# Kernel tuning notes

Measured on AMD Instinct MI355X. Metric: run time of the kernel, lower is better.

## Reference

```python
import math
import jax, jax.numpy as jnp
import numpy as np

IN_SIZE = 16
OUT_SIZE = 16
MIN_SCALE = 1e-3
CONST = 1000.0
DEFAULT_U_A = math.log(math.e - 1.0 - MIN_SCALE)
BATCH = 32768
N_PARAMS = OUT_SIZE ** 2 + 2 * OUT_SIZE + OUT_SIZE * IN_SIZE  # 544


def setup_inputs() -> dict:
    key = jax.random.key(0)
    kx, kh = jax.random.split(key)
    x = jax.random.normal(kx, (BATCH, IN_SIZE), dtype=jnp.float32)
    h = jax.random.normal(kh, (BATCH, N_PARAMS), dtype=jnp.float32)
    return {"x": x, "h": h}


def reference(x, h):
    B = h.shape[0]
    O, I = OUT_SIZE, IN_SIZE
    # extract_parameters
    da = h[:, :O]                                   # (B,O)
    db = h[:, O:2 * O]                              # (B,O)
    dw = h[:, 2 * O:2 * O + O * O].reshape(B, O, O)  # (B,O,O)
    du = h[:, 2 * O + O * O:].reshape(B, O, I)       # (B,O,I)

    u_pre = du / CONST
    u = jax.nn.softmax(u_pre, axis=-1)
    log_u = jax.nn.log_softmax(u_pre, axis=-1)
    a = jax.nn.softplus(DEFAULT_U_A + da / CONST) + MIN_SCALE
    b = db / CONST
    w_pre = dw / CONST
    w = jax.nn.softmax(w_pre, axis=-1)
    log_w = jax.nn.log_softmax(w_pre, axis=-1)

    # forward transform
    ux = jnp.einsum('boi,bi->bo', u, x)             # (B,O)
    c = jax.nn.sigmoid(a * ux + b)                  # (B,O)
    d = jnp.einsum('bij,bj->bi', w, c)              # (B,O)
    z = jnp.log(d / (1.0 - d))                      # inverse_sigmoid

    # log-space Jacobian: J = diag(1/(d(1-d))) @ W @ diag(sigma'(c)*a) @ U
    log_t1 = (jnp.log(d) - jnp.log(1.0 - d))[:, :, None]                  # (B,O,1)
    log_t3 = (jax.nn.log_sigmoid(c) + jax.nn.log_sigmoid(-c))[:, None, :]  # (B,1,O)
    log_t4 = jnp.log(a)[:, None, :]                                        # (B,1,O)
    m1 = (log_t1 + log_w + log_t3 + log_t4)[:, :, :, None]                 # (B,O,O,1)
    m2 = log_u[:, None, :, :]                                              # (B,1,O,I)
    # log_dot: logsumexp over the contraction dim (-2), keepdim
    log_jac = jax.scipy.special.logsumexp(m1 + m2, axis=-2, keepdims=True)  # (B,O,1,I)
    log_det = jnp.sum(log_jac, axis=(1, 2, 3))                              # (B,)
    return z, log_det


if __name__ == "__main__":
    out = reference(**setup_inputs())
    print(out[0].shape, out[1].shape)
```

## Files before the change

### kernel.cpp

```cpp
#include <hip/hip_runtime.h>

#define BATCH   32768
#define OSZ     16
#define ISZ     16
#define NP      544
#define EPB     16
#define HS      552
#define NF4     (EPB*NP/4)
#define ROWF4   (NP/4)

__global__ __launch_bounds__(256, 4)
void dsit_kernel(const float* __restrict__ x, const float* __restrict__ h,
                 float* __restrict__ out_z, float* __restrict__ out_ld) {
    __shared__ float h_s[EPB * HS];
    __shared__ float x_s[EPB * ISZ];
    __shared__ float c_s[EPB * OSZ];
    __shared__ float s_s[EPB * OSZ];

    const int tid = threadIdx.x;
    const int blk = blockIdx.x;

    {
        const float4* hg = (const float4*)(h + (size_t)blk * (EPB * NP));
        #pragma unroll
        for (int k = 0; k < 9; ++k) {
            int f4 = tid + (k << 8);
            if (f4 < NF4) {
                int e  = f4 / ROWF4;
                int c4 = f4 - e * ROWF4;
                ((float4*)h_s)[e * (HS / 4) + c4] = hg[f4];
            }
        }
        if (tid < (EPB * ISZ / 4)) {
            ((float4*)x_s)[tid] = ((const float4*)(x + (size_t)blk * (EPB * ISZ)))[tid];
        }
    }
    __syncthreads();

    const int e = tid >> 4;
    const int r = tid & 15;
    float* he = &h_s[e * HS];
    const float* xe = &x_s[e * ISZ];

    const float K = 1.0e-3f;
    const float u_a = logf(expf(1.0f) - 1.001f);

    float a  = log1pf(expf(u_a + he[r] * K)) + 1.0e-3f;
    float bb = he[OSZ + r] * K;

    float wrow[16];
    float wsum = 0.0f;
    #pragma unroll
    for (int j = 0; j < 16; ++j) {
        float v = __expf(he[32 + 16 * r + j] * K);
        wrow[j] = v; wsum += v;
    }
    float winv = 1.0f / wsum;
    #pragma unroll
    for (int j = 0; j < 16; ++j) wrow[j] *= winv;

    float urow[16];
    float usum = 0.0f;
    #pragma unroll
    for (int i = 0; i < 16; ++i) {
        float v = __expf(he[288 + 16 * r + i] * K);
        urow[i] = v; usum += v;
    }
    float uinv = 1.0f / usum;
    float ux = 0.0f;
    #pragma unroll
    for (int i = 0; i < 16; ++i) {
        urow[i] *= uinv;
        ux += urow[i] * xe[i];
    }
    #pragma unroll
    for (int i = 0; i < 16; ++i) he[288 + 16 * r + i] = urow[i];

    float cpre = a * ux + bb;
    float c  = 1.0f / (1.0f + __expf(-cpre));
    float sc = 1.0f / (1.0f + __expf(-c));
    float s  = sc * (1.0f - sc) * a;
    c_s[e * OSZ + r] = c;
    s_s[e * OSZ + r] = s;
    __syncthreads();

    float d = 0.0f;
    #pragma unroll
    for (int j = 0; j < 16; ++j) d += wrow[j] * c_s[e * OSZ + j];
    float z = logf(d) - logf(1.0f - d);
    out_z[(size_t)blk * 256 + tid] = z;

    #pragma unroll
    for (int j = 0; j < 16; ++j) wrow[j] *= s_s[e * OSZ + j];

    float acc[16];
    #pragma unroll
    for (int i = 0; i < 16; ++i) acc[i] = 0.0f;
    #pragma unroll
    for (int j = 0; j < 16; ++j) {
        float wj = wrow[j];
        const float* uj = &he[288 + 16 * j];
        #pragma unroll
        for (int i = 0; i < 16; ++i) acc[i] += wj * uj[i];
    }

    float partial = 16.0f * z;
    #pragma unroll
    for (int i = 0; i < 16; ++i) partial += logf(acc[i]);

    #pragma unroll
    for (int m = 1; m < 16; m <<= 1) partial += __shfl_xor(partial, m, 16);
    if (r == 0) out_ld[blk * EPB + e] = partial;
}

extern "C" void kernel_launch(void* const* d_in, const int* in_sizes, int n_in,
                              void* d_out, int out_size, void* d_ws, size_t ws_size,
                              hipStream_t stream) {
    const float* x = (const float*)d_in[0];
    const float* h = (const float*)d_in[1];
    float* out_z  = (float*)d_out;
    float* out_ld = out_z + (size_t)BATCH * OSZ;

    dim3 grid(BATCH / EPB);
    dim3 block(256);
    dsit_kernel<<<grid, block, 0, stream>>>(x, h, out_z, out_ld);
}
```

Measured before the change: 108.8 us.

## Load h rows straight from global into registers and shrink shared memory

Each thread now reads its own U and W rows from global memory as float4 loads into registers, where the old kernel first staged the whole 544-float parameter block in shared memory. Only the normalized U rows go to a smaller padded shared buffer, and c and s are packed into one float2 array. The Jacobian contraction reads U as float4 from shared memory, and the exact logf/log1pf calls are replaced with __logf. The aim is less shared-memory traffic and footprint, and higher occupancy. In exchange, the per-thread global loads are strided and not fully coalesced, and the fast log intrinsics are less accurate.

```diff
diff --git a/kernel.cpp b/kernel.cpp
--- a/kernel.cpp
+++ b/kernel.cpp
@@ -1,116 +1,106 @@
 #include <hip/hip_runtime.h>
 
-#define BATCH   32768
-#define OSZ     16
-#define ISZ     16
-#define NP      544
-#define EPB     16
-#define HS      552
-#define NF4     (EPB*NP/4)
-#define ROWF4   (NP/4)
+#define BATCH 32768
+#define EPB   16
+#define RS    20
+#define US    328
+#define CS    40
+#define XS    20
 
 __global__ __launch_bounds__(256, 4)
 void dsit_kernel(const float* __restrict__ x, const float* __restrict__ h,
                  float* __restrict__ out_z, float* __restrict__ out_ld) {
-    __shared__ float h_s[EPB * HS];
-    __shared__ float x_s[EPB * ISZ];
-    __shared__ float c_s[EPB * OSZ];
-    __shared__ float s_s[EPB * OSZ];
+    __shared__ float u_s[EPB * US];
+    __shared__ float cs_s[EPB * CS];
+    __shared__ float x_s[EPB * XS];
 
     const int tid = threadIdx.x;
     const int blk = blockIdx.x;
+    const int e = tid >> 4;
+    const int r = tid & 15;
 
-    {
-        const float4* hg = (const float4*)(h + (size_t)blk * (EPB * NP));
-        #pragma unroll
-        for (int k = 0; k < 9; ++k) {
-            int f4 = tid + (k << 8);
-            if (f4 < NF4) {
-                int e  = f4 / ROWF4;
-                int c4 = f4 - e * ROWF4;
-                ((float4*)h_s)[e * (HS / 4) + c4] = hg[f4];
-            }
-        }
-        if (tid < (EPB * ISZ / 4)) {
-            ((float4*)x_s)[tid] = ((const float4*)(x + (size_t)blk * (EPB * ISZ)))[tid];
-        }
+    if (tid < 64) {
+        float4 v = ((const float4*)(x + (size_t)blk * 256))[tid];
+        *(float4*)&x_s[(tid >> 2) * XS + ((tid & 3) << 2)] = v;
     }
+
+    const float* hb = h + (size_t)blk * (EPB * 544) + e * 544;
+    const float K   = 1.0e-3f;
+    const float U_A = 0.54074353f;
+
+    float da = hb[r];
+    float db = hb[16 + r];
+
+    float ur[16], wr[16];
+    *(float4*)&ur[0]  = *(const float4*)(hb + 288 + 16 * r);
+    *(float4*)&ur[4]  = *(const float4*)(hb + 288 + 16 * r + 4);
+    *(float4*)&ur[8]  = *(const float4*)(hb + 288 + 16 * r + 8);
+    *(float4*)&ur[12] = *(const float4*)(hb + 288 + 16 * r + 12);
+    *(float4*)&wr[0]  = *(const float4*)(hb + 32 + 16 * r);
+    *(float4*)&wr[4]  = *(const float4*)(hb + 32 + 16 * r + 4);
+    *(float4*)&wr[8]  = *(const float4*)(hb + 32 + 16 * r + 8);
+    *(float4*)&wr[12] = *(const float4*)(hb + 32 + 16 * r + 12);
+
+    float a  = __logf(1.0f + __expf(U_A + da * K)) + 1.0e-3f;
+    float bb = db * K;
+
+    float usum = 0.0f;
+    #pragma unroll
+    for (int i = 0; i < 16; ++i) { ur[i] = __expf(ur[i] * K); usum += ur[i]; }
+    float uinv = 1.0f / usum;
+
+    float wsum = 0.0f;
+    #pragma unroll
+    for (int j = 0; j < 16; ++j) { wr[j] = __expf(wr[j] * K); wsum += wr[j]; }
+    float winv = 1.0f / wsum;
+    #pragma unroll
+    for (int j = 0; j < 16; ++j) wr[j] *= winv;
+
     __syncthreads();
 
-    const int e = tid >> 4;
-    const int r = tid & 15;
-    float* he = &h_s[e * HS];
-    const float* xe = &x_s[e * ISZ];
-
-    const float K = 1.0e-3f;
-    const float u_a = logf(expf(1.0f) - 1.001f);
-
-    float a  = log1pf(expf(u_a + he[r] * K)) + 1.0e-3f;
-    float bb = he[OSZ + r] * K;
-
-    float wrow[16];
-    float wsum = 0.0f;
-    #pragma unroll
-    for (int j = 0; j < 16; ++j) {
-        float v = __expf(he[32 + 16 * r + j] * K);
-        wrow[j] = v; wsum += v;
-    }
-    float winv = 1.0f / wsum;
-    #pragma unroll
-    for (int j = 0; j < 16; ++j) wrow[j] *= winv;
-
-    float urow[16];
-    float usum = 0.0f;
-    #pragma unroll
-    for (int i = 0; i < 16; ++i) {
-        float v = __expf(he[288 + 16 * r + i] * K);
-        urow[i] = v; usum += v;
-    }
-    float uinv = 1.0f / usum;
     float ux = 0.0f;
     #pragma unroll
-    for (int i = 0; i < 16; ++i) {
-        urow[i] *= uinv;
-        ux += urow[i] * xe[i];
-    }
-    #pragma unroll
-    for (int i = 0; i < 16; ++i) he[288 + 16 * r + i] = urow[i];
+    for (int i = 0; i < 16; ++i) { ur[i] *= uinv; ux += ur[i] * x_s[e * XS + i]; }
+
+    *(float4*)&u_s[e * US + r * RS + 0]  = *(float4*)&ur[0];
+    *(float4*)&u_s[e * US + r * RS + 4]  = *(float4*)&ur[4];
+    *(float4*)&u_s[e * US + r * RS + 8]  = *(float4*)&ur[8];
+    *(float4*)&u_s[e * US + r * RS + 12] = *(float4*)&ur[12];
 
     float cpre = a * ux + bb;
     float c  = 1.0f / (1.0f + __expf(-cpre));
     float sc = 1.0f / (1.0f + __expf(-c));
     float s  = sc * (1.0f - sc) * a;
-    c_s[e * OSZ + r] = c;
-    s_s[e * OSZ + r] = s;
+    *(float2*)&cs_s[e * CS + 2 * r] = make_float2(c, s);
+
     __syncthreads();
 
     float d = 0.0f;
     #pragma unroll
-    for (int j = 0; j < 16; ++j) d += wrow[j] * c_s[e * OSZ + j];
-    float z = logf(d) - logf(1.0f - d);
+    for (int j = 0; j < 16; ++j) {
+        float2 cs = *(const float2*)&cs_s[e * CS + 2 * j];
+        d += wr[j] * cs.x;
+        wr[j] *= cs.y;
+    }
+    float z = __logf(d / (1.0f - d));
     out_z[(size_t)blk * 256 + tid] = z;
 
+    float part = 16.0f * z;
     #pragma unroll
-    for (int j = 0; j < 16; ++j) wrow[j] *= s_s[e * OSZ + j];
-
-    float acc[16];
-    #pragma unroll
-    for (int i = 0; i < 16; ++i) acc[i] = 0.0f;
-    #pragma unroll
-    for (int j = 0; j < 16; ++j) {
-        float wj = wrow[j];
-        const float* uj = &he[288 + 16 * j];
+    for (int i4 = 0; i4 < 4; ++i4) {
+        float ax = 0.f, ay = 0.f, az = 0.f, aw = 0.f;
         #pragma unroll
-        for (int i = 0; i < 16; ++i) acc[i] += wj * uj[i];
+        for (int j = 0; j < 16; ++j) {
+            float wj = wr[j];
+            float4 uq = *(const float4*)&u_s[e * US + j * RS + (i4 << 2)];
+            ax += wj * uq.x; ay += wj * uq.y; az += wj * uq.z; aw += wj * uq.w;
+        }
+        part += __logf(ax) + __logf(ay) + __logf(az) + __logf(aw);
     }
 
-    float partial = 16.0f * z;
     #pragma unroll
-    for (int i = 0; i < 16; ++i) partial += logf(acc[i]);
-
-    #pragma unroll
-    for (int m = 1; m < 16; m <<= 1) partial += __shfl_xor(partial, m, 16);
-    if (r == 0) out_ld[blk * EPB + e] = partial;
+    for (int m = 1; m < 16; m <<= 1) part += __shfl_xor(part, m, 16);
+    if (r == 0) out_ld[blk * EPB + e] = part;
 }
 
 extern "C" void kernel_launch(void* const* d_in, const int* in_sizes, int n_in,
@@ -119,9 +109,7 @@
     const float* x = (const float*)d_in[0];
     const float* h = (const float*)d_in[1];
     float* out_z  = (float*)d_out;
-    float* out_ld = out_z + (size_t)BATCH * OSZ;
+    float* out_ld = out_z + (size_t)BATCH * 16;
 
-    dim3 grid(BATCH / EPB);
-    dim3 block(256);
-    dsit_kernel<<<grid, block, 0, stream>>>(x, h, out_z, out_ld);
+    dsit_kernel<<<dim3(BATCH / EPB), dim3(256), 0, stream>>>(x, h, out_z, out_ld);
 }
```

New measurement: 102.0 us. 6.3% less time.
